# Kernel tuning notes

Measured on AMD Instinct MI355X. Metric: run time of the kernel, lower is better.

Reference implementation:

```python
import jax, jax.numpy as jnp
import numpy as np

EPS = 1e-5

def _ln(x, g, b):
    mu = x.mean(-1, keepdims=True)
    var = ((x - mu) ** 2).mean(-1, keepdims=True)
    return (x - mu) * jax.lax.rsqrt(var + EPS) * g + b

def setup_inputs() -> dict:
    B, K, D, H, T = 64, 64, 128, 128, 4
    key = jax.random.key(0)
    ks = jax.random.split(key, 20)
    s = 0.02
    inp = {
        "slots": jax.random.normal(ks[0], (B, K, D), jnp.float32),
        "edge_probs": jax.random.uniform(ks[1], (B, K, K), jnp.float32),
        "edge_types": jax.random.uniform(ks[2], (B, K, K, T), jnp.float32),
        # f_self: LayerNorm(D) -> Linear(D,H) -> ReLU -> Linear(H,D)
        "ls_g": jnp.ones((D,), jnp.float32),
        "ls_b": jnp.zeros((D,), jnp.float32),
        "ws1": jax.random.normal(ks[3], (D, H), jnp.float32) * s,
        "bs1": jnp.zeros((H,), jnp.float32),
        "ws2": jax.random.normal(ks[4], (H, D), jnp.float32) * s,
        "bs2": jnp.zeros((D,), jnp.float32),
        # f_inter[tau]: Linear(2D,H) -> ReLU -> Linear(H,H) -> ReLU -> Linear(H,D), stacked over T
        "wi1": jax.random.normal(ks[5], (T, 2 * D, H), jnp.float32) * s,
        "bi1": jnp.zeros((T, H), jnp.float32),
        "wi2": jax.random.normal(ks[6], (T, H, H), jnp.float32) * s,
        "bi2": jnp.zeros((T, H), jnp.float32),
        "wi3": jax.random.normal(ks[7], (T, H, D), jnp.float32) * s,
        "bi3": jnp.zeros((T, D), jnp.float32),
        # update_mlp: LayerNorm(2D) -> Linear(2D,H) -> ReLU -> Linear(H,D)
        "lu_g": jnp.ones((2 * D,), jnp.float32),
        "lu_b": jnp.zeros((2 * D,), jnp.float32),
        "wu1": jax.random.normal(ks[8], (2 * D, H), jnp.float32) * s,
        "bu1": jnp.zeros((H,), jnp.float32),
        "wu2": jax.random.normal(ks[9], (H, D), jnp.float32) * s,
        "bu2": jnp.zeros((D,), jnp.float32),
    }
    return inp

NUM_MP = 2

def reference(slots, edge_probs, edge_types, ls_g, ls_b, ws1, bs1, ws2, bs2,
              wi1, bi1, wi2, bi2, wi3, bi3, lu_g, lu_b, wu1, bu1, wu2, bu2):
    B, K, D = slots.shape
    T = edge_types.shape[-1]
    h = slots
    for _ in range(NUM_MP):
        # f_self
        delta_self = jax.nn.relu(_ln(h, ls_g, ls_b) @ ws1 + bs1) @ ws2 + bs2
        # all-pairs features: cat[b,i,j] = [h[b,i] (sender), h[b,j] (receiver)]
        sender = jnp.broadcast_to(h[:, :, None, :], (B, K, K, D))
        receiver = jnp.broadcast_to(h[:, None, :, :], (B, K, K, D))
        pair = jnp.concatenate([sender, receiver], axis=-1)  # [B,K,K,2D]
        delta_inter = jnp.zeros_like(h)
        for tau in range(T):
            x = jax.nn.relu(pair @ wi1[tau] + bi1[tau])
            x = jax.nn.relu(x @ wi2[tau] + bi2[tau])
            eff = x @ wi3[tau] + bi3[tau]  # [B,K,K,D]
            w = edge_probs[..., None] * edge_types[..., tau, None]  # [B,K,K,1]
            delta_inter = delta_inter + (eff * w).sum(axis=1)  # sum over sender i
        combined = jnp.concatenate([h + delta_self, delta_inter], axis=-1)
        update = jax.nn.relu(_ln(combined, lu_g, lu_b) @ wu1 + bu1) @ wu2 + bu2
        h = h + update  # residual=True
    return h
```

## Files before the change

kernel.cpp:

```cpp
#include <hip/hip_runtime.h>
#include <hip/hip_fp16.h>

#define BATCH 64
#define KSLOT 64
#define DDIM  128
#define HDIM  128
#define TTYPE 4
#define NSLOT (BATCH*KSLOT)
#define EPSLN 1e-5f
#define YROW  544

typedef _Float16 v8h __attribute__((ext_vector_type(8)));
typedef _Float16 v4h __attribute__((ext_vector_type(4)));
typedef _Float16 v2h __attribute__((ext_vector_type(2)));
typedef float    v4f __attribute__((ext_vector_type(4)));

__device__ __forceinline__ float waveAllSum(float v) {
    #pragma unroll
    for (int m = 1; m < 64; m <<= 1) v += __shfl_xor(v, m, 64);
    return v;
}

__global__ __launch_bounds__(256) void k_wconv(
        const float* __restrict__ ws1, const float* __restrict__ wi1,
        const float* __restrict__ ws2, const float* __restrict__ wu1,
        const float* __restrict__ wu2, const float* __restrict__ wi3,
        const float* __restrict__ wi2, const float* __restrict__ bi1,
        const float* __restrict__ bi3,
        const float* __restrict__ ep, const float* __restrict__ et,
        __half* __restrict__ ws1T, __half* __restrict__ wi1catT,
        __half* __restrict__ ws2T, __half* __restrict__ wu1T,
        __half* __restrict__ wu2T, __half* __restrict__ w3catT,
        __half* __restrict__ w2T16, float* __restrict__ biascat,
        __half* __restrict__ wPre) {
    __shared__ __align__(16) float tile[128*132];
    int bx = blockIdx.x, tid = threadIdx.x;
    if (bx >= 22) {
        int bx2 = bx - 22, b = bx2 >> 2, chunk = bx2 & 3;
        const float4* etb = (const float4*)(et + (size_t)b*16384);
        const float*  epb = ep + (size_t)b*4096;
        __half* w0 = wPre + ((size_t)0*BATCH + b)*4096;
        __half* w1 = wPre + ((size_t)1*BATCH + b)*4096;
        __half* w2 = wPre + ((size_t)2*BATCH + b)*4096;
        __half* w3 = wPre + ((size_t)3*BATCH + b)*4096;
        int c0 = chunk*1024;
        for (int c = c0 + tid; c < c0 + 1024; c += 256) {
            float wv = epb[c];
            float4 e = etb[c];
            w0[c] = __float2half(wv * e.x);
            w1[c] = __float2half(wv * e.y);
            w2[c] = __float2half(wv * e.z);
            w3[c] = __float2half(wv * e.w);
        }
        return;
    }
    if (bx == 21) {
        for (int idx = tid; idx < 128*32; idx += 256) {
            int o = idx >> 5, c = idx & 31;
            w3catT[(size_t)o*YROW + 512 + c] = (c < 4) ? __float2half(bi3[c*DDIM + o]) : __float2half(0.f);
        }
        for (int idx = tid; idx < 1024; idx += 256) {
            int th = idx >> 7, o = idx & 127;
            biascat[idx] = (th & 1) ? bi1[(th>>1)*HDIM + o] : 0.f;
        }
        return;
    }
    const float* src; __half* dst; int dstride = 128, dcol = 0;
    if (bx == 0)      { src = ws1; dst = ws1T; }
    else if (bx <= 8) { int th = bx-1, tau = th>>1, half = th&1;
                        src = wi1 + ((size_t)tau*256 + half*128)*128;
                        dst = wi1catT + (size_t)th*128*128; }
    else if (bx == 9) { src = ws2; dst = ws2T; }
    else if (bx ==10) { src = wu2; dst = wu2T; }
    else if (bx <=12) { int hh = bx-11; src = wu1 + (size_t)hh*128*128;
                        dst = wu1T; dstride = 256; dcol = hh*128; }
    else if (bx <=16) { int tau = bx-13; src = wi3 + (size_t)tau*16384;
                        dst = w3catT; dstride = YROW; dcol = tau*128; }
    else              { int tau = bx-17; src = wi2 + (size_t)tau*16384;
                        dst = w2T16 + (size_t)tau*16384; }
    for (int idx = tid; idx < 4096; idx += 256) {
        int r = idx >> 5, c4 = idx & 31;
        *(float4*)&tile[r*132 + c4*4] = *(const float4*)&src[(size_t)r*128 + c4*4];
    }
    __syncthreads();
    for (int idx = tid; idx < 8192; idx += 256) {
        int n = idx >> 6, kp = idx & 63;
        __half2 p = __floats2half2_rn(tile[(2*kp)*132 + n], tile[(2*kp+1)*132 + n]);
        *(__half2*)&dst[(size_t)n*dstride + dcol + 2*kp] = p;
    }
}

#define LROW 136
__global__ __launch_bounds__(512) void k_pair(
        const float* __restrict__ h,
        const __half* __restrict__ wi1catT,
        const float* __restrict__ biascat,
        const __half* __restrict__ w2T16,
        const float* __restrict__ bi2,
        const __half* __restrict__ wPre,
        __half* __restrict__ Ycat) {
    __shared__ __align__(16) _Float16 w2T[HDIM*LROW];
    __shared__ __align__(16) _Float16 Cs[KSLOT*LROW];
    __shared__ __align__(16) _Float16 As[KSLOT*LROW];
    __shared__ __align__(16) _Float16 wS[KSLOT*KSLOT];
    __shared__ __align__(16) _Float16 hs[KSLOT*136];
    int bx = blockIdx.x, b = bx >> 2, tau = bx & 3;
    int tid = threadIdx.x, lane = tid & 63, w = tid >> 6;
    int jt = w >> 1, oh = w & 1, quad = lane >> 4, n = lane & 15;

    for (int idx = tid; idx < 2048; idx += 512) {
        int o = idx >> 4, seg = (idx & 15)*8;
        *(v8h*)&w2T[o*LROW + seg] = *(const v8h*)&w2T16[((size_t)tau*128 + o)*128 + seg];
    }
    {
        int row = tid >> 3, c0 = (tid & 7)*16;
        const float* hp = &h[(size_t)(b*KSLOT + row)*128 + c0];
        #pragma unroll
        for (int q = 0; q < 4; q++) {
            float4 f = *(const float4*)&hp[q*4];
            *(__half2*)&hs[row*136 + c0 + q*4]     = __floats2half2_rn(f.x, f.y);
            *(__half2*)&hs[row*136 + c0 + q*4 + 2] = __floats2half2_rn(f.z, f.w);
        }
    }
    {
        int base = tid*8;
        *(v8h*)&wS[base] = *(const v8h*)&wPre[((size_t)tau*BATCH + b)*4096 + base];
    }
    __syncthreads();

    {
        int hf = w >> 2, rt = w & 3;
        const __half* wb = wi1catT + (size_t)(tau*2 + hf)*128*128;
        const float* bcp = biascat + (tau*2 + hf)*128;
        _Float16* dst = hf ? Cs : As;
        v8h afr[4];
        #pragma unroll
        for (int ks = 0; ks < 4; ks++)
            afr[ks] = *(const v8h*)&hs[(rt*16 + n)*136 + ks*32 + quad*8];
        #pragma unroll
        for (int ot = 0; ot < 8; ot++) {
            float b0 = bcp[ot*16 + n];
            v4f acc = (v4f){b0, b0, b0, b0};
            #pragma unroll
            for (int ks = 0; ks < 4; ks++)
                acc = __builtin_amdgcn_mfma_f32_16x16x32_f16(
                    afr[ks], *(const v8h*)&wb[(size_t)(ot*16 + n)*128 + ks*32 + quad*8], acc, 0, 0, 0);
            #pragma unroll
            for (int r = 0; r < 4; r++)
                dst[(rt*16 + quad*4 + r)*LROW + ot*16 + n] = (_Float16)acc[r];
        }
    }
    __syncthreads();

    v8h bfrag[4][4];
    #pragma unroll
    for (int ot = 0; ot < 4; ot++)
        #pragma unroll
        for (int ks = 0; ks < 4; ks++)
            bfrag[ot][ks] = *(const v8h*)&w2T[(oh*64 + ot*16 + n)*LROW + ks*32 + quad*8];
    v8h cfrag[4];
    #pragma unroll
    for (int ks = 0; ks < 4; ks++)
        cfrag[ks] = *(const v8h*)&Cs[(jt*16 + n)*LROW + ks*32 + quad*8];
    v4f biasvec[4];
    #pragma unroll
    for (int ot = 0; ot < 4; ot++) {
        float b0 = bi2[tau*HDIM + oh*64 + ot*16 + n];
        biasvec[ot] = (v4f){b0, b0, b0, b0};
    }

    v4h yacch[4];
    #pragma unroll
    for (int ot = 0; ot < 4; ot++) yacch[ot] = (v4h){0,0,0,0};
    v4h wsacch = (v4h){0,0,0,0};
    const v8h zero8 = {0,0,0,0,0,0,0,0};
    const v4h zero4h = {0,0,0,0};

    v8h aN[4]; v4h wvN;
    #pragma unroll
    for (int ks = 0; ks < 4; ks++) aN[ks] = *(const v8h*)&As[ks*32 + quad*8];
    wvN = *(const v4h*)&wS[jt*16 + quad*4];

    for (int i = 0; i < KSLOT; ++i) {
        v8h a[4]; v4h wv = wvN;
        #pragma unroll
        for (int ks = 0; ks < 4; ks++) a[ks] = aN[ks];
        if (i < KSLOT-1) {
            #pragma unroll
            for (int ks = 0; ks < 4; ks++)
                aN[ks] = *(const v8h*)&As[(i+1)*LROW + ks*32 + quad*8];
            wvN = *(const v4h*)&wS[(i+1)*KSLOT + jt*16 + quad*4];
        }
        v8h x1[4];
        #pragma unroll
        for (int ks = 0; ks < 4; ks++)
            x1[ks] = __builtin_elementwise_max(a[ks] + cfrag[ks], zero8);
        v4f acc0 = biasvec[0], acc1 = biasvec[1], acc2 = biasvec[2], acc3 = biasvec[3];
        #pragma unroll
        for (int ks = 0; ks < 4; ks++) {
            acc0 = __builtin_amdgcn_mfma_f32_16x16x32_f16(x1[ks], bfrag[0][ks], acc0, 0, 0, 0);
            acc1 = __builtin_amdgcn_mfma_f32_16x16x32_f16(x1[ks], bfrag[1][ks], acc1, 0, 0, 0);
            acc2 = __builtin_amdgcn_mfma_f32_16x16x32_f16(x1[ks], bfrag[2][ks], acc2, 0, 0, 0);
            acc3 = __builtin_amdgcn_mfma_f32_16x16x32_f16(x1[ks], bfrag[3][ks], acc3, 0, 0, 0);
        }
        #define EPI(ACC, OT) { \
            v2h lo = __builtin_bit_cast(v2h, __builtin_amdgcn_cvt_pkrtz(ACC[0], ACC[1])); \
            v2h hi = __builtin_bit_cast(v2h, __builtin_amdgcn_cvt_pkrtz(ACC[2], ACC[3])); \
            v4h rel = {lo[0], lo[1], hi[0], hi[1]}; \
            rel = __builtin_elementwise_max(rel, zero4h); \
            yacch[OT] = yacch[OT] + wv * rel; }
        EPI(acc0, 0) EPI(acc1, 1) EPI(acc2, 2) EPI(acc3, 3)
        #undef EPI
        wsacch = wsacch + wv;
    }

    #pragma unroll
    for (int r = 0; r < 4; r++) {
        int j = jt*16 + quad*4 + r;
        __half* yb = Ycat + (size_t)(b*KSLOT + j)*YROW + tau*128 + oh*64;
        #pragma unroll
        for (int ot = 0; ot < 4; ot++)
            yb[ot*16 + n] = __float2half((float)yacch[ot][r]);
    }
    if (oh == 0 && n == 0) {
        #pragma unroll
        for (int r = 0; r < 4; r++)
            Ycat[(size_t)(b*KSLOT + jt*16 + quad*4 + r)*YROW + 512 + tau] = __float2half((float)wsacch[r]);
    }
    if (tau == 0 && oh == 1 && n == 0) {
        const v4h z4 = {0,0,0,0};
        #pragma unroll
        for (int r = 0; r < 4; r++) {
            _Float16* pz = (_Float16*)(Ycat + (size_t)(b*KSLOT + jt*16 + quad*4 + r)*YROW + 516);
            #pragma unroll
            for (int c = 0; c < 28; c += 4) *(v4h*)&pz[c] = z4;
        }
    }
}

__global__ __launch_bounds__(512, 2) void k_mega(
        const __half* __restrict__ Ycat, const __half* __restrict__ w3catT,
        const float* __restrict__ ls_g, const float* __restrict__ ls_b,
        const __half* __restrict__ ws1T, const float* __restrict__ bs1,
        const __half* __restrict__ ws2T, const float* __restrict__ bs2,
        const float* __restrict__ g, const float* __restrict__ bb,
        const __half* __restrict__ wu1T, const float* __restrict__ bu1,
        const __half* __restrict__ wu2T, const float* __restrict__ bu2,
        const float* __restrict__ h, float* __restrict__ hout) {
    __shared__ __align__(16) _Float16 Ys[16*552];
    __shared__ __align__(16) float    Crow[16*260];
    __shared__ __align__(16) float    Hrow[16*132];
    __shared__ __align__(16) _Float16 Xs[16*136];
    __shared__ __align__(16) _Float16 Ts[16*136];
    __shared__ __align__(16) _Float16 Xa[16*264];
    __shared__ __align__(16) _Float16 Ut[16*136];
    int tid = threadIdx.x, lane = tid & 63, w = tid >> 6;
    int n = lane & 15, quad = lane >> 4;
    int row0 = blockIdx.x*16;

    for (int u = tid; u < 1024; u += 512) {
        int r = u >> 6, seg = (u & 63)*8;
        *(v8h*)&Ys[r*552 + seg] = *(const v8h*)&Ycat[(size_t)(row0 + r)*YROW + seg];
    }
    if (tid < 64) {
        int r = tid >> 2, seg = 512 + (tid & 3)*8;
        *(v8h*)&Ys[r*552 + seg] = *(const v8h*)&Ycat[(size_t)(row0 + r)*YROW + seg];
    }
    {
        int r = tid >> 5, c4 = (tid & 31)*4;
        *(float4*)&Hrow[r*132 + c4] = *(const float4*)&h[(size_t)(row0 + r)*128 + c4];
    }
    __syncthreads();
    {
        const __half* wp = w3catT + (size_t)(w*16 + n)*YROW + quad*8;
        const _Float16* yp = &Ys[n*552 + quad*8];
        v4f acc = (v4f){0.f,0.f,0.f,0.f};
        #pragma unroll 4
        for (int ks = 0; ks < 17; ks++) {
            v8h a  = *(const v8h*)(yp + ks*32);
            v8h bf = *(const v8h*)(wp + ks*32);
            acc = __builtin_amdgcn_mfma_f32_16x16x32_f16(a, bf, acc, 0, 0, 0);
        }
        #pragma unroll
        for (int r = 0; r < 4; r++)
            Crow[(quad*4 + r)*260 + 128 + w*16 + n] = acc[r];
    }
    #pragma unroll
    for (int rr = 0; rr < 2; rr++) {
        int r = w*2 + rr;
        float x0 = Hrow[r*132 + 2*lane], x1 = Hrow[r*132 + 2*lane + 1];
        float mu = waveAllSum(x0 + x1) * (1.f/128.f);
        float d0 = x0 - mu, d1 = x1 - mu;
        float var = waveAllSum(d0*d0 + d1*d1) * (1.f/128.f);
        float rs = rsqrtf(var + EPSLN);
        float2 gv = *(const float2*)&ls_g[2*lane];
        float2 bv = *(const float2*)&ls_b[2*lane];
        *(__half2*)&Xs[r*136 + 2*lane] = __floats2half2_rn(d0*rs*gv.x + bv.x, d1*rs*gv.y + bv.y);
    }
    __syncthreads();
    {
        float b0 = bs1[w*16 + n];
        v4f acc = (v4f){b0, b0, b0, b0};
        const __half* wp = ws1T + (size_t)(w*16 + n)*128 + quad*8;
        #pragma unroll
        for (int ks = 0; ks < 4; ks++) {
            v8h a  = *(const v8h*)&Xs[n*136 + ks*32 + quad*8];
            v8h bf = *(const v8h*)(wp + ks*32);
            acc = __builtin_amdgcn_mfma_f32_16x16x32_f16(a, bf, acc, 0, 0, 0);
        }
        #pragma unroll
        for (int r = 0; r < 4; r++)
            Ts[(quad*4 + r)*136 + w*16 + n] = (_Float16)fmaxf(acc[r], 0.f);
    }
    __syncthreads();
    {
        float b0 = bs2[w*16 + n];
        v4f acc = (v4f){b0, b0, b0, b0};
        const __half* wp = ws2T + (size_t)(w*16 + n)*128 + quad*8;
        #pragma unroll
        for (int ks = 0; ks < 4; ks++) {
            v8h a  = *(const v8h*)&Ts[n*136 + ks*32 + quad*8];
            v8h bf = *(const v8h*)(wp + ks*32);
            acc = __builtin_amdgcn_mfma_f32_16x16x32_f16(a, bf, acc, 0, 0, 0);
        }
        #pragma unroll
        for (int r = 0; r < 4; r++) {
            int rr = quad*4 + r, col = w*16 + n;
            Crow[rr*260 + col] = Hrow[rr*132 + col] + acc[r];
        }
    }
    __syncthreads();
    #pragma unroll
    for (int rr = 0; rr < 2; rr++) {
        int r = w*2 + rr;
        float4 v = *(const float4*)&Crow[r*260 + 4*lane];
        float mu = waveAllSum(v.x + v.y + v.z + v.w) * (1.f/256.f);
        float d0 = v.x-mu, d1 = v.y-mu, d2 = v.z-mu, d3 = v.w-mu;
        float var = waveAllSum(d0*d0 + d1*d1 + d2*d2 + d3*d3) * (1.f/256.f);
        float rs = rsqrtf(var + EPSLN);
        float4 gv = *(const float4*)&g[4*lane];
        float4 bv = *(const float4*)&bb[4*lane];
        *(__half2*)&Xa[r*264 + 4*lane]     = __floats2half2_rn(d0*rs*gv.x + bv.x, d1*rs*gv.y + bv.y);
        *(__half2*)&Xa[r*264 + 4*lane + 2] = __floats2half2_rn(d2*rs*gv.z + bv.z, d3*rs*gv.w + bv.w);
    }
    __syncthreads();
    {
        float b0 = bu1[w*16 + n];
        v4f acc = (v4f){b0, b0, b0, b0};
        const __half* wp = wu1T + (size_t)(w*16 + n)*256 + quad*8;
        const _Float16* xp = &Xa[n*264 + quad*8];
        #pragma unroll 4
        for (int ks = 0; ks < 8; ks++) {
            v8h a  = *(const v8h*)(xp + ks*32);
            v8h bf = *(const v8h*)(wp + ks*32);
            acc = __builtin_amdgcn_mfma_f32_16x16x32_f16(a, bf, acc, 0, 0, 0);
        }
        #pragma unroll
        for (int r = 0; r < 4; r++)
            Ut[(quad*4 + r)*136 + w*16 + n] = (_Float16)fmaxf(acc[r], 0.f);
    }
    __syncthreads();
    {
        float b0 = bu2[w*16 + n];
        v4f acc = (v4f){b0, b0, b0, b0};
        const __half* wp = wu2T + (size_t)(w*16 + n)*128 + quad*8;
        #pragma unroll
        for (int ks = 0; ks < 4; ks++) {
            v8h a  = *(const v8h*)&Ut[n*136 + ks*32 + quad*8];
            v8h bf = *(const v8h*)(wp + ks*32);
            acc = __builtin_amdgcn_mfma_f32_16x16x32_f16(a, bf, acc, 0, 0, 0);
        }
        #pragma unroll
        for (int r = 0; r < 4; r++) {
            int rr = quad*4 + r, col = w*16 + n;
            hout[(size_t)(row0 + rr)*128 + col] = Hrow[rr*132 + col] + acc[r];
        }
    }
}

extern "C" void kernel_launch(void* const* d_in, const int* in_sizes, int n_in,
                              void* d_out, int out_size, void* d_ws, size_t ws_size,
                              hipStream_t stream) {
    const float* slots = (const float*)d_in[0];
    const float* ep    = (const float*)d_in[1];
    const float* et    = (const float*)d_in[2];
    const float* ls_g  = (const float*)d_in[3];
    const float* ls_b  = (const float*)d_in[4];
    const float* ws1   = (const float*)d_in[5];
    const float* bs1   = (const float*)d_in[6];
    const float* ws2   = (const float*)d_in[7];
    const float* bs2   = (const float*)d_in[8];
    const float* wi1   = (const float*)d_in[9];
    const float* bi1   = (const float*)d_in[10];
    const float* wi2   = (const float*)d_in[11];
    const float* bi2   = (const float*)d_in[12];
    const float* wi3   = (const float*)d_in[13];
    const float* bi3   = (const float*)d_in[14];
    const float* lu_g  = (const float*)d_in[15];
    const float* lu_b  = (const float*)d_in[16];
    const float* wu1   = (const float*)d_in[17];
    const float* bu1   = (const float*)d_in[18];
    const float* wu2   = (const float*)d_in[19];
    const float* bu2   = (const float*)d_in[20];
    float* out = (float*)d_out;

    char* p = (char*)d_ws;
    float*  h_buf   = (float*)p;   p += (size_t)NSLOT*DDIM*4;
    __half* Ycat    = (__half*)p;  p += (size_t)NSLOT*YROW*2;
    __half* wPre    = (__half*)p;  p += (size_t)TTYPE*BATCH*4096*2;
    __half* ws1T    = (__half*)p;  p += 128*128*2;
    __half* wi1catT = (__half*)p;  p += 1024*128*2;
    __half* ws2T    = (__half*)p;  p += 128*128*2;
    __half* wu1T    = (__half*)p;  p += 128*256*2;
    __half* wu2T    = (__half*)p;  p += 128*128*2;
    __half* w3catT  = (__half*)p;  p += 128*YROW*2;
    __half* w2T16   = (__half*)p;  p += 4*128*128*2;
    float*  biascat = (float*)p;   p += 1024*4;

    k_wconv<<<22 + 256, 256, 0, stream>>>(ws1, wi1, ws2, wu1, wu2, wi3, wi2, bi1, bi3,
                                          ep, et, ws1T, wi1catT, ws2T, wu1T, wu2T,
                                          w3catT, w2T16, biascat, wPre);

    for (int mp = 0; mp < 2; mp++) {
        const float* h = (mp == 0) ? slots : h_buf;
        float* hout = (mp == 0) ? h_buf : out;
        k_pair<<<BATCH*TTYPE, 512, 0, stream>>>(h, wi1catT, biascat, w2T16, bi2, wPre, Ycat);
        k_mega<<<NSLOT/16, 512, 0, stream>>>(Ycat, w3catT, ls_g, ls_b, ws1T, bs1, ws2T, bs2,
                                             lu_g, lu_b, wu1T, bu1, wu2T, bu2, h, hout);
    }
}
```

Baseline: 200.8 us.

## Stream layer-2 weights from LDS and alias h buffer to raise occupancy

The k_pair kernel stops keeping the 16 layer-2 weight fragments in registers and now reads them from shared memory inside the inner loop. It also drops the next-iteration prefetch of A and edge weights, and sets launch bounds to 4 blocks per CU. The h staging buffer now shares space with the w2 weight buffer, which is loaded after the first GEMM behind an extra barrier, so the LDS footprint shrinks. The aim is more resident waves per CU through fewer VGPRs and less LDS, at the cost of many more LDS reads per MFMA and less latency hiding inside each wave.

```diff
diff --git a/kernel.cpp b/kernel.cpp
--- a/kernel.cpp
+++ b/kernel.cpp
@@ -91,7 +91,7 @@
 }
 
 #define LROW 136
-__global__ __launch_bounds__(512) void k_pair(
+__global__ __launch_bounds__(512, 4) void k_pair(
         const float* __restrict__ h,
         const __half* __restrict__ wi1catT,
         const float* __restrict__ biascat,
@@ -99,27 +99,22 @@
         const float* __restrict__ bi2,
         const __half* __restrict__ wPre,
         __half* __restrict__ Ycat) {
-    __shared__ __align__(16) _Float16 w2T[HDIM*LROW];
+    __shared__ __align__(16) _Float16 U[HDIM*LROW];
     __shared__ __align__(16) _Float16 Cs[KSLOT*LROW];
     __shared__ __align__(16) _Float16 As[KSLOT*LROW];
     __shared__ __align__(16) _Float16 wS[KSLOT*KSLOT];
-    __shared__ __align__(16) _Float16 hs[KSLOT*136];
     int bx = blockIdx.x, b = bx >> 2, tau = bx & 3;
     int tid = threadIdx.x, lane = tid & 63, w = tid >> 6;
     int jt = w >> 1, oh = w & 1, quad = lane >> 4, n = lane & 15;
 
-    for (int idx = tid; idx < 2048; idx += 512) {
-        int o = idx >> 4, seg = (idx & 15)*8;
-        *(v8h*)&w2T[o*LROW + seg] = *(const v8h*)&w2T16[((size_t)tau*128 + o)*128 + seg];
-    }
     {
         int row = tid >> 3, c0 = (tid & 7)*16;
         const float* hp = &h[(size_t)(b*KSLOT + row)*128 + c0];
         #pragma unroll
         for (int q = 0; q < 4; q++) {
             float4 f = *(const float4*)&hp[q*4];
-            *(__half2*)&hs[row*136 + c0 + q*4]     = __floats2half2_rn(f.x, f.y);
-            *(__half2*)&hs[row*136 + c0 + q*4 + 2] = __floats2half2_rn(f.z, f.w);
+            *(__half2*)&U[row*LROW + c0 + q*4]     = __floats2half2_rn(f.x, f.y);
+            *(__half2*)&U[row*LROW + c0 + q*4 + 2] = __floats2half2_rn(f.z, f.w);
         }
     }
     {
@@ -136,7 +131,7 @@
         v8h afr[4];
         #pragma unroll
         for (int ks = 0; ks < 4; ks++)
-            afr[ks] = *(const v8h*)&hs[(rt*16 + n)*136 + ks*32 + quad*8];
+            afr[ks] = *(const v8h*)&U[(rt*16 + n)*LROW + ks*32 + quad*8];
         #pragma unroll
         for (int ot = 0; ot < 8; ot++) {
             float b0 = bcp[ot*16 + n];
@@ -151,13 +146,14 @@
         }
     }
     __syncthreads();
-
-    v8h bfrag[4][4];
-    #pragma unroll
-    for (int ot = 0; ot < 4; ot++)
-        #pragma unroll
-        for (int ks = 0; ks < 4; ks++)
-            bfrag[ot][ks] = *(const v8h*)&w2T[(oh*64 + ot*16 + n)*LROW + ks*32 + quad*8];
+    #pragma unroll
+    for (int k2 = 0; k2 < 4; k2++) {
+        int idx = tid + k2*512;
+        int o = idx >> 4, seg = (idx & 15)*8;
+        *(v8h*)&U[o*LROW + seg] = *(const v8h*)&w2T16[((size_t)tau*128 + o)*128 + seg];
+    }
+    __syncthreads();
+
     v8h cfrag[4];
     #pragma unroll
     for (int ks = 0; ks < 4; ks++)
@@ -176,21 +172,14 @@
     const v8h zero8 = {0,0,0,0,0,0,0,0};
     const v4h zero4h = {0,0,0,0};
 
-    v8h aN[4]; v4h wvN;
-    #pragma unroll
-    for (int ks = 0; ks < 4; ks++) aN[ks] = *(const v8h*)&As[ks*32 + quad*8];
-    wvN = *(const v4h*)&wS[jt*16 + quad*4];
+    const _Float16* ub = &U[(oh*64 + n)*LROW + quad*8];
 
     for (int i = 0; i < KSLOT; ++i) {
-        v8h a[4]; v4h wv = wvN;
-        #pragma unroll
-        for (int ks = 0; ks < 4; ks++) a[ks] = aN[ks];
-        if (i < KSLOT-1) {
-            #pragma unroll
-            for (int ks = 0; ks < 4; ks++)
-                aN[ks] = *(const v8h*)&As[(i+1)*LROW + ks*32 + quad*8];
-            wvN = *(const v4h*)&wS[(i+1)*KSLOT + jt*16 + quad*4];
-        }
+        v8h a[4];
+        #pragma unroll
+        for (int ks = 0; ks < 4; ks++)
+            a[ks] = *(const v8h*)&As[i*LROW + ks*32 + quad*8];
+        v4h wv = *(const v4h*)&wS[i*KSLOT + jt*16 + quad*4];
         v8h x1[4];
         #pragma unroll
         for (int ks = 0; ks < 4; ks++)
@@ -198,10 +187,10 @@
         v4f acc0 = biasvec[0], acc1 = biasvec[1], acc2 = biasvec[2], acc3 = biasvec[3];
         #pragma unroll
         for (int ks = 0; ks < 4; ks++) {
-            acc0 = __builtin_amdgcn_mfma_f32_16x16x32_f16(x1[ks], bfrag[0][ks], acc0, 0, 0, 0);
-            acc1 = __builtin_amdgcn_mfma_f32_16x16x32_f16(x1[ks], bfrag[1][ks], acc1, 0, 0, 0);
-            acc2 = __builtin_amdgcn_mfma_f32_16x16x32_f16(x1[ks], bfrag[2][ks], acc2, 0, 0, 0);
-            acc3 = __builtin_amdgcn_mfma_f32_16x16x32_f16(x1[ks], bfrag[3][ks], acc3, 0, 0, 0);
+            acc0 = __builtin_amdgcn_mfma_f32_16x16x32_f16(x1[ks], *(const v8h*)(ub + 0*16*LROW + ks*32), acc0, 0, 0, 0);
+            acc1 = __builtin_amdgcn_mfma_f32_16x16x32_f16(x1[ks], *(const v8h*)(ub + 1*16*LROW + ks*32), acc1, 0, 0, 0);
+            acc2 = __builtin_amdgcn_mfma_f32_16x16x32_f16(x1[ks], *(const v8h*)(ub + 2*16*LROW + ks*32), acc2, 0, 0, 0);
+            acc3 = __builtin_amdgcn_mfma_f32_16x16x32_f16(x1[ks], *(const v8h*)(ub + 3*16*LROW + ks*32), acc3, 0, 0, 0);
         }
         #define EPI(ACC, OT) { \
             v2h lo = __builtin_bit_cast(v2h, __builtin_amdgcn_cvt_pkrtz(ACC[0], ACC[1])); \
```

New measurement: 223.0 us. 11.1% more time.
